# Performance work log

Measured on AMD Instinct MI355X. Metric: run time of the kernel, lower is better.

The kernel has to match this reference:

```python
import jax, jax.numpy as jnp
import numpy as np

EMB = 1024
HEADS = 16
HEAD_DIM = EMB // HEADS


def setup_inputs() -> dict:
    key = jax.random.key(0)
    ks = jax.random.split(key, 9)
    s = 1.0 / np.sqrt(EMB)
    x = jax.random.normal(ks[0], (2, 2048, EMB), dtype=jnp.float32)
    Wq = jax.random.normal(ks[1], (EMB, EMB), dtype=jnp.float32) * s
    bq = jnp.zeros((EMB,), dtype=jnp.float32)
    Wk = jax.random.normal(ks[2], (EMB, EMB), dtype=jnp.float32) * s
    bk = jnp.zeros((EMB,), dtype=jnp.float32)
    Wv = jax.random.normal(ks[3], (EMB, EMB), dtype=jnp.float32) * s
    bv = jnp.zeros((EMB,), dtype=jnp.float32)
    Wo = jax.random.normal(ks[4], (EMB, EMB), dtype=jnp.float32) * s
    bo = jnp.zeros((EMB,), dtype=jnp.float32)
    return {"x": x, "Wq": Wq, "bq": bq, "Wk": Wk, "bk": bk,
            "Wv": Wv, "bv": bv, "Wo": Wo, "bo": bo}


def reference(x, Wq, bq, Wk, bk, Wv, bv, Wo, bo):
    B, S, E = x.shape
    # torch Linear: y = x @ W.T + b
    q = x @ Wq.T + bq
    k = x @ Wk.T + bk
    v = x @ Wv.T + bv
    # [B,S,E] -> [B,H,S,D]
    q = q.reshape(B, S, HEADS, HEAD_DIM).transpose(0, 2, 1, 3)
    k = k.reshape(B, S, HEADS, HEAD_DIM).transpose(0, 2, 1, 3)
    v = v.reshape(B, S, HEADS, HEAD_DIM).transpose(0, 2, 1, 3)
    energy = jnp.einsum('bhqd,bhkd->bhqk', q, k)
    scaling = jnp.float32(E) ** 0.5  # NOTE: sqrt(emb_size), not sqrt(head_dim), as in source
    att = jax.nn.softmax(energy / scaling, axis=-1)
    out = jnp.einsum('bhqk,bhkd->bhqd', att, v)
    out = out.transpose(0, 2, 1, 3).reshape(B, S, E)
    return out @ Wo.T + bo
```

## Files before the change

kernel.cpp:

```cpp
#include <hip/hip_runtime.h>
#include <stdint.h>


typedef _Float16 half8  __attribute__((ext_vector_type(8)));
typedef _Float16 half4v __attribute__((ext_vector_type(4)));
typedef _Float16 half2v __attribute__((ext_vector_type(2)));
typedef float    f32x4  __attribute__((ext_vector_type(4)));
typedef float    f32x16 __attribute__((ext_vector_type(16)));

#define GLD16(g, l) __builtin_amdgcn_global_load_lds(                         \
    (__attribute__((address_space(1))) void*)(g),                            \
    (__attribute__((address_space(3))) void*)(l), 16, 0, 0)

#define MFMA16(a, b, c) __builtin_amdgcn_mfma_f32_16x16x32_f16((a), (b), (c), 0, 0, 0)
#define MFMA32(a, b, c) __builtin_amdgcn_mfma_f32_32x32x16_f16((a), (b), (c), 0, 0, 0)

#if __has_builtin(__builtin_amdgcn_exp2f)
#define EXP2(x) __builtin_amdgcn_exp2f(x)
#else
#define EXP2(x) exp2f(x)
#endif

static __device__ inline uint32_t pk_u32(float a, float b)
{
    auto t = __builtin_amdgcn_cvt_pkrtz(a, b);
    return __builtin_bit_cast(uint32_t, t);
}

__global__ void cvt_all(const float* __restrict__ x,  const float* __restrict__ wq,
                        const float* __restrict__ wk, const float* __restrict__ wv,
                        const float* __restrict__ wo, _Float16* __restrict__ xb,
                        _Float16* __restrict__ wqkv, _Float16* __restrict__ wob)
{
    int i = blockIdx.x * blockDim.x + threadIdx.x;
    const float* src; _Float16* dst; int off;
    if (i < 1048576)      { src = x;  dst = xb;                 off = i; }
    else if (i < 1310720) { src = wq; dst = wqkv;               off = i - 1048576; }
    else if (i < 1572864) { src = wk; dst = wqkv + 1048576;     off = i - 1310720; }
    else if (i < 1835008) { src = wv; dst = wqkv + 2097152;     off = i - 1572864; }
    else                  { src = wo; dst = wob;                off = i - 1835008; }
    float4 f = ((const float4*)src)[off];
    half4v h = { (_Float16)f.x, (_Float16)f.y, (_Float16)f.z, (_Float16)f.w };
    ((half4v*)dst)[off] = h;
}

template<int BN, int MODE>
__global__ __launch_bounds__(256, MODE == 0 ? 3 : 2)
void gemm_f16(const _Float16* __restrict__ A, const _Float16* __restrict__ W,
              const float* __restrict__ b0, const float* __restrict__ b1,
              const float* __restrict__ b2, _Float16* __restrict__ o0,
              _Float16* __restrict__ o1, _Float16* __restrict__ o2,
              float* __restrict__ outf, float qscale)
{
    constexpr int NI = BN / 32;
    __shared__ _Float16 lA[128 * 64];
    __shared__ _Float16 lB[BN * 64];
    const int m0 = blockIdx.y * 128, n0 = blockIdx.x * BN;
    const int tid = threadIdx.x, lane = tid & 63, w = tid >> 6;
    const int wr = (w >> 1) * 64, wc = (w & 1) * (BN / 2);
    const int lrow = lane & 15, lk4 = lane >> 4;
    f32x4 acc[4][NI] = {};

    for (int k0 = 0; k0 < 1024; k0 += 64) {
        __syncthreads();
#pragma unroll
        for (int c = 0; c < 4; ++c) {
            int sidx = c * 256 + tid;
            int row = sidx >> 3, sl = sidx & 7;
            int gc = k0 + ((sl ^ (row & 7)) << 3);
            GLD16(A + (size_t)(m0 + row) * 1024 + gc, lA + (size_t)(c * 256 + w * 64) * 8);
        }
#pragma unroll
        for (int c = 0; c < BN / 32; ++c) {
            int sidx = c * 256 + tid;
            int row = sidx >> 3, sl = sidx & 7;
            int gc = k0 + ((sl ^ (row & 7)) << 3);
            GLD16(W + (size_t)(n0 + row) * 1024 + gc, lB + (size_t)(c * 256 + w * 64) * 8);
        }
        __syncthreads();

#pragma unroll
        for (int kd = 0; kd < 2; ++kd) {
            half8 af[4], bf[NI];
#pragma unroll
            for (int mi = 0; mi < 4; ++mi) {
                int ra = wr + mi * 16 + lrow;
                af[mi] = *(const half8*)(lA + ra * 64 + (((kd * 4 + lk4) ^ (ra & 7)) * 8));
            }
#pragma unroll
            for (int ni = 0; ni < NI; ++ni) {
                int rb = wc + ni * 16 + lrow;
                bf[ni] = *(const half8*)(lB + rb * 64 + (((kd * 4 + lk4) ^ (rb & 7)) * 8));
            }
#pragma unroll
            for (int mi = 0; mi < 4; ++mi)
#pragma unroll
                for (int ni = 0; ni < NI; ++ni)
                    acc[mi][ni] = MFMA16(af[mi], bf[ni], acc[mi][ni]);
        }
    }

    if (MODE == 0) {
        const int which = n0 >> 10;
        const float* bp = which == 0 ? b0 : which == 1 ? b1 : b2;
        const float scale = which == 0 ? qscale : 1.f;
        const int nh = n0 & 1023;
        float bcol[NI];
#pragma unroll
        for (int ni = 0; ni < NI; ++ni) bcol[ni] = bp[nh + wc + ni * 16 + lrow];
        if (which == 2) {
#pragma unroll
            for (int mi = 0; mi < 4; ++mi)
#pragma unroll
                for (int ni = 0; ni < NI; ++ni) {
                    int cg = nh + wc + ni * 16 + lrow;
                    int hh = cg >> 6, dd = cg & 63;
                    int sb = m0 + wr + mi * 16 + lk4 * 4;
                    int bb = sb >> 11, ss = sb & 2047;
                    half4v pkv;
#pragma unroll
                    for (int r = 0; r < 4; ++r)
                        pkv[r] = (_Float16)(acc[mi][ni][r] + bcol[ni]);
                    *(half4v*)(o2 + ((size_t)(bb * 16 + hh) * 64 + dd) * 2048 + ss) = pkv;
                }
        } else {
            _Float16* outh = which == 0 ? o0 : o1;
#pragma unroll
            for (int mi = 0; mi < 4; ++mi)
#pragma unroll
                for (int ni = 0; ni < NI; ++ni)
#pragma unroll
                    for (int r = 0; r < 4; ++r) {
                        int rg = m0 + wr + mi * 16 + lk4 * 4 + r;
                        int cg = nh + wc + ni * 16 + lrow;
                        float v = (acc[mi][ni][r] + bcol[ni]) * scale;
                        int b = rg >> 11, s = rg & 2047, hh = cg >> 6, dd = cg & 63;
                        outh[(((size_t)b * 16 + hh) * 2048 + s) * 64 + dd] = (_Float16)v;
                    }
        }
    } else {
        float bcol[NI];
#pragma unroll
        for (int ni = 0; ni < NI; ++ni) bcol[ni] = b0[n0 + wc + ni * 16 + lrow];
#pragma unroll
        for (int mi = 0; mi < 4; ++mi)
#pragma unroll
            for (int ni = 0; ni < NI; ++ni)
#pragma unroll
                for (int r = 0; r < 4; ++r) {
                    int rg = m0 + wr + mi * 16 + lk4 * 4 + r;
                    int cg = n0 + wc + ni * 16 + lrow;
                    outf[(size_t)rg * 1024 + cg] = acc[mi][ni][r] + bcol[ni];
                }
    }
}

#define KVB 64
#define NT  32
__global__ __launch_bounds__(256, 2)
void attn(const _Float16* __restrict__ q, const _Float16* __restrict__ k,
          const _Float16* __restrict__ vt, _Float16* __restrict__ ao)
{
    __shared__ _Float16 lKf[3 * KVB * 64];
    __shared__ _Float16 lVf[3 * 64 * KVB];
    const int bid0 = blockIdx.x;
    const int bid = (bid0 & 7) * 64 + (bid0 >> 3);
    const int bh = bid >> 4, q0 = (bid & 15) * 128;
    const int bb = bh >> 4, hh = bh & 15;
    const int tid = threadIdx.x, lane = tid & 63, w = tid >> 6;
    const int l31 = lane & 31, h = lane >> 5;
    const _Float16* qh = q + (size_t)bh * 2048 * 64;
    const _Float16* kh = k + (size_t)bh * 2048 * 64;
    const _Float16* vth = vt + (size_t)bh * 64 * 2048;

    half8 qf[4];
#pragma unroll
    for (int kd = 0; kd < 4; ++kd)
        qf[kd] = *(const half8*)(qh + (size_t)(q0 + w * 32 + l31) * 64
                                    + kd * 16 + h * 8);

    float l_ = 0.f;
    f32x16 o0 = {}, o1 = {};

    auto STAGE = [&](int t, int bs) {
        const int s0 = t * KVB;
        _Float16* Kd = lKf + bs * (KVB * 64);
        _Float16* Vd = lVf + bs * (64 * KVB);
#pragma unroll
        for (int c = 0; c < 2; ++c) {
            int sidx = c * 256 + tid;
            int row = sidx >> 3, sl = sidx & 7;
            GLD16(kh + (size_t)(s0 + row) * 64 + ((sl ^ (row & 7)) * 8),
                  Kd + (size_t)(c * 256 + w * 64) * 8);
            GLD16(vth + (size_t)row * 2048 + s0 + ((sl ^ (row & 7)) * 8),
                  Vd + (size_t)(c * 256 + w * 64) * 8);
        }
    };

    STAGE(0, 0);
    STAGE(1, 1);

    for (int t = 0; t < NT; ++t) {
        const int cur = t % 3;
        if (t < NT - 1) asm volatile("s_waitcnt vmcnt(4)" ::: "memory");
        else            asm volatile("s_waitcnt vmcnt(0)" ::: "memory");
        __builtin_amdgcn_s_barrier();
        __builtin_amdgcn_sched_barrier(0);
        if (t + 2 < NT) STAGE(t + 2, (t + 2) % 3);

        const _Float16* Kb = lKf + cur * (KVB * 64);
        const _Float16* Vb = lVf + cur * (64 * KVB);

        half8 kf[8], vf[8];
#pragma unroll
        for (int kd = 0; kd < 4; ++kd) {
            int s0l = (kd * 2 + h) ^ (l31 & 7);
            int s1l = (kd * 2 + h) ^ ((32 + l31) & 7);
            kf[kd * 2]     = *(const half8*)(Kb + l31 * 64 + s0l * 8);
            kf[kd * 2 + 1] = *(const half8*)(Kb + (32 + l31) * 64 + s1l * 8);
        }
#pragma unroll
        for (int ks = 0; ks < 4; ++ks) {
            int s0l = (ks * 2 + h) ^ (l31 & 7);
            int s1l = (ks * 2 + h) ^ ((32 + l31) & 7);
            vf[ks * 2]     = *(const half8*)(Vb + l31 * 64 + s0l * 8);
            vf[ks * 2 + 1] = *(const half8*)(Vb + (32 + l31) * 64 + s1l * 8);
        }

        f32x16 e0 = {}, e1 = {};
        __builtin_amdgcn_s_setprio(1);
#pragma unroll
        for (int kd = 0; kd < 4; ++kd) {
            e0 = MFMA32(kf[kd * 2], qf[kd], e0);
            e1 = MFMA32(kf[kd * 2 + 1], qf[kd], e1);
        }
        __builtin_amdgcn_s_setprio(0);

        half8 pa[4];
        {
            float p[16];
#pragma unroll
            for (int r = 0; r < 16; ++r) p[r] = EXP2(e0[r]);
            l_ += (((p[0] + p[1]) + (p[2] + p[3])) + ((p[4] + p[5]) + (p[6] + p[7])))
                + (((p[8] + p[9]) + (p[10] + p[11])) + ((p[12] + p[13]) + (p[14] + p[15])));
#pragma unroll
            for (int bq = 0; bq < 2; ++bq) {
                uint32_t w0 = pk_u32(p[bq * 8 + 0], p[bq * 8 + 1]);
                uint32_t w1 = pk_u32(p[bq * 8 + 2], p[bq * 8 + 3]);
                uint32_t w2 = pk_u32(p[bq * 8 + 4], p[bq * 8 + 5]);
                uint32_t w3 = pk_u32(p[bq * 8 + 6], p[bq * 8 + 7]);
                asm volatile("v_permlane32_swap_b32 %0, %1" : "+v"(w0), "+v"(w2));
                asm volatile("v_permlane32_swap_b32 %0, %1" : "+v"(w1), "+v"(w3));
                union { uint32_t u[4]; half8 hv; } uu;
                uu.u[0] = w0; uu.u[1] = w1; uu.u[2] = w2; uu.u[3] = w3;
                pa[bq] = uu.hv;
            }
        }

        __builtin_amdgcn_s_setprio(1);
#pragma unroll
        for (int ks = 0; ks < 2; ++ks) {
            o0 = MFMA32(pa[ks], vf[ks * 2], o0);
            o1 = MFMA32(pa[ks], vf[ks * 2 + 1], o1);
        }
        __builtin_amdgcn_s_setprio(0);

        {
            float p[16];
#pragma unroll
            for (int r = 0; r < 16; ++r) p[r] = EXP2(e1[r]);
            l_ += (((p[0] + p[1]) + (p[2] + p[3])) + ((p[4] + p[5]) + (p[6] + p[7])))
                + (((p[8] + p[9]) + (p[10] + p[11])) + ((p[12] + p[13]) + (p[14] + p[15])));
#pragma unroll
            for (int bq = 0; bq < 2; ++bq) {
                uint32_t w0 = pk_u32(p[bq * 8 + 0], p[bq * 8 + 1]);
                uint32_t w1 = pk_u32(p[bq * 8 + 2], p[bq * 8 + 3]);
                uint32_t w2 = pk_u32(p[bq * 8 + 4], p[bq * 8 + 5]);
                uint32_t w3 = pk_u32(p[bq * 8 + 6], p[bq * 8 + 7]);
                asm volatile("v_permlane32_swap_b32 %0, %1" : "+v"(w0), "+v"(w2));
                asm volatile("v_permlane32_swap_b32 %0, %1" : "+v"(w1), "+v"(w3));
                union { uint32_t u[4]; half8 hv; } uu;
                uu.u[0] = w0; uu.u[1] = w1; uu.u[2] = w2; uu.u[3] = w3;
                pa[2 + bq] = uu.hv;
            }
        }

        __builtin_amdgcn_s_setprio(1);
#pragma unroll
        for (int ks = 2; ks < 4; ++ks) {
            o0 = MFMA32(pa[ks], vf[ks * 2], o0);
            o1 = MFMA32(pa[ks], vf[ks * 2 + 1], o1);
        }
        __builtin_amdgcn_s_setprio(0);
    }

    l_ += __shfl_xor(l_, 32);
    const size_t obase = ((size_t)bb * 2048) * 1024 + hh * 64;
#pragma unroll
    for (int r = 0; r < 16; ++r) {
        int qr = (r & 3) + 8 * (r >> 2) + 4 * h;
        float linv = 1.f / __shfl(l_, qr);
        int sg = q0 + w * 32 + qr;
        ao[obase + (size_t)sg * 1024 + l31]      = (_Float16)(o0[r] * linv);
        ao[obase + (size_t)sg * 1024 + 32 + l31] = (_Float16)(o1[r] * linv);
    }
}

extern "C" void kernel_launch(void* const* d_in, const int* in_sizes, int n_in,
                              void* d_out, int out_size, void* d_ws, size_t ws_size,
                              hipStream_t stream)
{
    const float* x  = (const float*)d_in[0];
    const float* Wq = (const float*)d_in[1];
    const float* bq = (const float*)d_in[2];
    const float* Wk = (const float*)d_in[3];
    const float* bk = (const float*)d_in[4];
    const float* Wv = (const float*)d_in[5];
    const float* bv = (const float*)d_in[6];
    const float* Wo = (const float*)d_in[7];
    const float* bo = (const float*)d_in[8];
    float* out = (float*)d_out;

    char* ws = (char*)d_ws;
    _Float16* xb   = (_Float16*)(ws);
    _Float16* aob  = xb;
    _Float16* wqkv = (_Float16*)(ws + (8u  << 20));
    _Float16* wob  = (_Float16*)(ws + (14u << 20));
    _Float16* qb   = (_Float16*)(ws + (16u << 20));
    _Float16* kb   = (_Float16*)(ws + (24u << 20));
    _Float16* vtb  = (_Float16*)(ws + (32u << 20));

    cvt_all<<<8192, 256, 0, stream>>>(x, Wq, Wk, Wv, Wo, xb, wqkv, wob);

    const float qscale = 1.4426950408889634f / 32.f;
    gemm_f16<128, 0><<<dim3(24, 32), 256, 0, stream>>>(
        xb, wqkv, bq, bk, bv, qb, kb, vtb, nullptr, qscale);

    attn<<<512, 256, 0, stream>>>(qb, kb, vtb, aob);

    gemm_f16<64, 1><<<dim3(16, 32), 256, 0, stream>>>(
        aob, wob, bo, nullptr, nullptr, nullptr, nullptr, nullptr, out, 1.f);
}
```

Measured before the change: 106.4 us.

## Pre-swizzle V into MFMA fragment layout and load directly to registers

The QKV GEMM epilogue now writes V in a tiled layout that matches the attention kernel's MFMA B-operand fragments, so each lane reads contiguous 16-byte chunks per tile. The attention kernel drops the V shared-memory staging and instead double-buffers V fragments in registers (vfA/vfB), prefetching two tiles ahead. The K swizzle in LDS also changes to a rotation scheme. This removes LDS traffic and bank-conflict work for V, at the cost of more VGPRs and longer-latency global loads in the loop.

```diff
diff --git a/kernel.cpp b/kernel.cpp
--- a/kernel.cpp
+++ b/kernel.cpp
@@ -4,7 +4,6 @@
 
 typedef _Float16 half8  __attribute__((ext_vector_type(8)));
 typedef _Float16 half4v __attribute__((ext_vector_type(4)));
-typedef _Float16 half2v __attribute__((ext_vector_type(2)));
 typedef float    f32x4  __attribute__((ext_vector_type(4)));
 typedef float    f32x16 __attribute__((ext_vector_type(16)));
 
@@ -117,11 +116,17 @@
                     int hh = cg >> 6, dd = cg & 63;
                     int sb = m0 + wr + mi * 16 + lk4 * 4;
                     int bb = sb >> 11, ss = sb & 2047;
+                    int tile = ss >> 6, ks = (ss >> 4) & 3;
+                    int hb = (ss >> 3) & 1, j0 = ss & 7;
+                    int c2 = dd >> 5, l31v = dd & 31;
                     half4v pkv;
 #pragma unroll
                     for (int r = 0; r < 4; ++r)
                         pkv[r] = (_Float16)(acc[mi][ni][r] + bcol[ni]);
-                    *(half4v*)(o2 + ((size_t)(bb * 16 + hh) * 64 + dd) * 2048 + ss) = pkv;
+                    size_t off = (size_t)(bb * 16 + hh) * 131072
+                               + tile * 4096 + (ks * 2 + c2) * 512
+                               + hb * 256 + l31v * 8 + j0;
+                    *(half4v*)(o2 + off) = pkv;
                 }
         } else {
             _Float16* outh = which == 0 ? o0 : o1;
@@ -159,19 +164,19 @@
 #define NT  32
 __global__ __launch_bounds__(256, 2)
 void attn(const _Float16* __restrict__ q, const _Float16* __restrict__ k,
-          const _Float16* __restrict__ vt, _Float16* __restrict__ ao)
+          const _Float16* __restrict__ vtf, _Float16* __restrict__ ao)
 {
     __shared__ _Float16 lKf[3 * KVB * 64];
-    __shared__ _Float16 lVf[3 * 64 * KVB];
     const int bid0 = blockIdx.x;
     const int bid = (bid0 & 7) * 64 + (bid0 >> 3);
     const int bh = bid >> 4, q0 = (bid & 15) * 128;
     const int bb = bh >> 4, hh = bh & 15;
     const int tid = threadIdx.x, lane = tid & 63, w = tid >> 6;
     const int l31 = lane & 31, h = lane >> 5;
+    const int kbase = (l31 & 7) + 2 * (l31 >> 3);
     const _Float16* qh = q + (size_t)bh * 2048 * 64;
     const _Float16* kh = k + (size_t)bh * 2048 * 64;
-    const _Float16* vth = vt + (size_t)bh * 64 * 2048;
+    const _Float16* vth = vtf + (size_t)bh * 131072;
 
     half8 qf[4];
 #pragma unroll
@@ -181,50 +186,46 @@
 
     float l_ = 0.f;
     f32x16 o0 = {}, o1 = {};
-
-    auto STAGE = [&](int t, int bs) {
+    half8 vfA[8], vfB[8];
+
+    auto STAGEK = [&](int t, int bs) {
         const int s0 = t * KVB;
         _Float16* Kd = lKf + bs * (KVB * 64);
-        _Float16* Vd = lVf + bs * (64 * KVB);
 #pragma unroll
         for (int c = 0; c < 2; ++c) {
-            int sidx = c * 256 + tid;
-            int row = sidx >> 3, sl = sidx & 7;
-            GLD16(kh + (size_t)(s0 + row) * 64 + ((sl ^ (row & 7)) * 8),
-                  Kd + (size_t)(c * 256 + w * 64) * 8);
-            GLD16(vth + (size_t)row * 2048 + s0 + ((sl ^ (row & 7)) * 8),
-                  Vd + (size_t)(c * 256 + w * 64) * 8);
+            int p = c * 256 + tid;
+            int r = p >> 3, jj = p & 7;
+            int col = (jj - (r & 7) - 2 * (r >> 3)) & 7;
+            GLD16(kh + (size_t)(s0 + r) * 64 + col * 8, Kd + (size_t)p * 8);
         }
     };
-
-    STAGE(0, 0);
-    STAGE(1, 1);
-
-    for (int t = 0; t < NT; ++t) {
-        const int cur = t % 3;
-        if (t < NT - 1) asm volatile("s_waitcnt vmcnt(4)" ::: "memory");
+    auto LOADV = [&](int t, half8 (&dst)[8]) {
+        const _Float16* src = vth + (size_t)t * 4096 + lane * 8;
+#pragma unroll
+        for (int i = 0; i < 8; ++i)
+            dst[i] = *(const half8*)(src + i * 512);
+    };
+
+    STAGEK(0, 0);
+    LOADV(0, vfA);
+    STAGEK(1, 1);
+    LOADV(1, vfB);
+
+    auto TILE = [&](int t, int bs, half8 (&vcur)[8]) {
+        if (t < NT - 1) asm volatile("s_waitcnt vmcnt(10)" ::: "memory");
         else            asm volatile("s_waitcnt vmcnt(0)" ::: "memory");
         __builtin_amdgcn_s_barrier();
         __builtin_amdgcn_sched_barrier(0);
-        if (t + 2 < NT) STAGE(t + 2, (t + 2) % 3);
-
-        const _Float16* Kb = lKf + cur * (KVB * 64);
-        const _Float16* Vb = lVf + cur * (64 * KVB);
-
-        half8 kf[8], vf[8];
+        int bs2 = bs + 2; if (bs2 >= 3) bs2 -= 3;
+        if (t + 2 < NT) STAGEK(t + 2, bs2);
+
+        const _Float16* Kb = lKf + bs * (KVB * 64);
+        half8 kf[8];
 #pragma unroll
         for (int kd = 0; kd < 4; ++kd) {
-            int s0l = (kd * 2 + h) ^ (l31 & 7);
-            int s1l = (kd * 2 + h) ^ ((32 + l31) & 7);
-            kf[kd * 2]     = *(const half8*)(Kb + l31 * 64 + s0l * 8);
-            kf[kd * 2 + 1] = *(const half8*)(Kb + (32 + l31) * 64 + s1l * 8);
-        }
-#pragma unroll
-        for (int ks = 0; ks < 4; ++ks) {
-            int s0l = (ks * 2 + h) ^ (l31 & 7);
-            int s1l = (ks * 2 + h) ^ ((32 + l31) & 7);
-            vf[ks * 2]     = *(const half8*)(Vb + l31 * 64 + s0l * 8);
-            vf[ks * 2 + 1] = *(const half8*)(Vb + (32 + l31) * 64 + s1l * 8);
+            int jj = (2 * kd + h + kbase) & 7;
+            kf[kd * 2]     = *(const half8*)(Kb + l31 * 64 + jj * 8);
+            kf[kd * 2 + 1] = *(const half8*)(Kb + (32 + l31) * 64 + jj * 8);
         }
 
         f32x16 e0 = {}, e1 = {};
@@ -258,11 +259,10 @@
         }
 
         __builtin_amdgcn_s_setprio(1);
-#pragma unroll
-        for (int ks = 0; ks < 2; ++ks) {
-            o0 = MFMA32(pa[ks], vf[ks * 2], o0);
-            o1 = MFMA32(pa[ks], vf[ks * 2 + 1], o1);
-        }
+        o0 = MFMA32(pa[0], vcur[0], o0);
+        o1 = MFMA32(pa[0], vcur[1], o1);
+        o0 = MFMA32(pa[1], vcur[2], o0);
+        o1 = MFMA32(pa[1], vcur[3], o1);
         __builtin_amdgcn_s_setprio(0);
 
         {
@@ -286,12 +286,21 @@
         }
 
         __builtin_amdgcn_s_setprio(1);
-#pragma unroll
-        for (int ks = 2; ks < 4; ++ks) {
-            o0 = MFMA32(pa[ks], vf[ks * 2], o0);
-            o1 = MFMA32(pa[ks], vf[ks * 2 + 1], o1);
-        }
+        o0 = MFMA32(pa[2], vcur[4], o0);
+        o1 = MFMA32(pa[2], vcur[5], o1);
+        o0 = MFMA32(pa[3], vcur[6], o0);
+        o1 = MFMA32(pa[3], vcur[7], o1);
         __builtin_amdgcn_s_setprio(0);
+
+        if (t + 2 < NT) LOADV(t + 2, vcur);
+    };
+
+    int cur = 0;
+    for (int t = 0; t < NT; t += 2) {
+        TILE(t, cur, vfA);
+        int c1 = cur + 1; if (c1 >= 3) c1 -= 3;
+        TILE(t + 1, c1, vfB);
+        cur += 2; if (cur >= 3) cur -= 3;
     }
 
     l_ += __shfl_xor(l_, 32);
@@ -328,15 +337,15 @@
     _Float16* wob  = (_Float16*)(ws + (14u << 20));
     _Float16* qb   = (_Float16*)(ws + (16u << 20));
     _Float16* kb   = (_Float16*)(ws + (24u << 20));
-    _Float16* vtb  = (_Float16*)(ws + (32u << 20));
+    _Float16* vtf  = (_Float16*)(ws + (32u << 20));
 
     cvt_all<<<8192, 256, 0, stream>>>(x, Wq, Wk, Wv, Wo, xb, wqkv, wob);
 
     const float qscale = 1.4426950408889634f / 32.f;
     gemm_f16<128, 0><<<dim3(24, 32), 256, 0, stream>>>(
-        xb, wqkv, bq, bk, bv, qb, kb, vtb, nullptr, qscale);
-
-    attn<<<512, 256, 0, stream>>>(qb, kb, vtb, aob);
+        xb, wqkv, bq, bk, bv, qb, kb, vtf, nullptr, qscale);
+
+    attn<<<512, 256, 0, stream>>>(qb, kb, vtf, aob);
 
     gemm_f16<64, 1><<<dim3(16, 32), 256, 0, stream>>>(
         aob, wob, bo, nullptr, nullptr, nullptr, nullptr, nullptr, out, 1.f);
```

Result: slower. 109.5 us (+2.9%).
